# Optimization experiments

Measured on AMD Instinct MI355X. Metric: run time of the kernel, lower is better.

## Reference

```python
import jax, jax.numpy as jnp
import numpy as np

N_NODES = 100000
N_EDGES = 1600000
D_FEAT = 64


def setup_inputs() -> dict:
    key = jax.random.key(0)
    k1, k2 = jax.random.split(key)
    x = jax.random.normal(k1, (N_NODES, D_FEAT), dtype=jnp.float32)
    edge_index = jax.random.randint(k2, (2, N_EDGES), 0, N_NODES, dtype=jnp.int64)
    return {"x": x, "edge_index": edge_index}


def reference(x, edge_index):
    # LGConv with normalize=True: out = D^{-1/2} A D^{-1/2} x
    src, dst = edge_index[0], edge_index[1]
    n = x.shape[0]
    # in-degree at destination nodes
    deg = jax.ops.segment_sum(jnp.ones_like(dst, dtype=x.dtype), dst, num_segments=n)
    deg_inv_sqrt = jnp.where(deg > 0, jax.lax.rsqrt(jnp.maximum(deg, 1.0)), 0.0)
    # per-edge normalization, gather-scale-scatter
    norm = deg_inv_sqrt[src] * deg_inv_sqrt[dst]  # [E]
    msgs = x[src] * norm[:, None]                 # [E, D]
    out = jax.ops.segment_sum(msgs, dst, num_segments=n)  # [N, D]
    return out
```

## Files before the change

kernel.cpp:

```cpp
#include <hip/hip_runtime.h>
#include <hip/hip_fp16.h>


#define DFEAT 64
#define BIN_W 391
#define TILE 8192
#define K1_THREADS 256
#define EPT (TILE / K1_THREADS)
#define DIRW 257
#define K3_THREADS 1024
#define MAX_NT 512
#define CAP 8192

typedef unsigned long long u64;
typedef unsigned int u32;
typedef float f4v __attribute__((ext_vector_type(4)));

__global__ __launch_bounds__(K1_THREADS)
void bin_kernel(const int* __restrict__ src, const int* __restrict__ dst,
                u32* __restrict__ records, int* __restrict__ dir,
                int* __restrict__ bin_cnt, int E, int N) {
    __shared__ int cnt[256];
    __shared__ int off[DIRW];
    __shared__ int rnk[256];
    __shared__ u32 buf[TILE];

    const int t    = blockIdx.x;
    const int base = t * TILE;
    const int tid  = threadIdx.x;

    cnt[tid] = 0;
    rnk[tid] = 0;
    __syncthreads();

    u32 rec[EPT];
    int myb[EPT];
    #pragma unroll
    for (int i = 0; i < EPT; ++i) {
        int e = base + tid + i * K1_THREADS;
        int b = -1;
        u32 r = 0;
        if (e < E) {
            unsigned d = (unsigned)dst[e];
            unsigned s = (unsigned)src[e];
            if (d < (unsigned)N && s < (unsigned)N) {
                b = (int)(d / BIN_W);
                r = ((d - (unsigned)b * BIN_W) << 23) | s;
            }
        }
        myb[i] = b;
        rec[i] = r;
        if (b >= 0) atomicAdd(&cnt[b], 1);
    }
    __syncthreads();

    int v = cnt[tid];
    off[tid] = v;
    __syncthreads();
    for (int d = 1; d < 256; d <<= 1) {
        int add = (tid >= d) ? off[tid - d] : 0;
        __syncthreads();
        off[tid] += add;
        __syncthreads();
    }
    int incl = off[tid];
    __syncthreads();
    off[tid] = incl - v;
    if (tid == 255) off[256] = incl;
    __syncthreads();

    dir[t * DIRW + tid] = off[tid];
    if (tid == 0) dir[t * DIRW + 256] = off[256];
    if (v > 0) atomicAdd(&bin_cnt[tid], v);

    #pragma unroll
    for (int i = 0; i < EPT; ++i) {
        int b = myb[i];
        if (b >= 0) {
            int r = atomicAdd(&rnk[b], 1);
            buf[off[b] + r] = rec[i];
        }
    }
    __syncthreads();

    int total = off[256];
    for (int i = tid; i < total; i += K1_THREADS)
        records[(size_t)base + i] = buf[i];
}

__global__ __launch_bounds__(K3_THREADS)
void csr_build_kernel(const u32* __restrict__ records,
                      const int* __restrict__ dir,
                      const int* __restrict__ bin_cnt,
                      float* __restrict__ dis,
                      int* __restrict__ row_ptr,
                      int* __restrict__ csr_src, int N, int NT, int NB,
                      int bshift, int nbuckets) {
    __shared__ u32 ldsrec[CAP];
    __shared__ int deg[512];
    __shared__ int cur[BIN_W];
    __shared__ int sbeg[MAX_NT];
    __shared__ int send[MAX_NT];
    __shared__ int lofs[MAX_NT];
    __shared__ int sh_total, sh_gb0;

    const int b  = blockIdx.x;
    const int lo = b * BIN_W;
    const int nodes = min(BIN_W, N - lo);
    const int tid = threadIdx.x;
    const int wave = tid >> 6, lane = tid & 63;

    int bv = 0;
    if (tid < 512) { bv = (tid < NB) ? bin_cnt[tid] : 0; deg[tid] = bv; }
    __syncthreads();
    for (int d = 1; d < 512; d <<= 1) {
        int a = (tid < 512 && tid >= d) ? deg[tid - d] : 0;
        __syncthreads();
        if (tid < 512) deg[tid] += a;
        __syncthreads();
    }
    if (tid == b) sh_gb0 = deg[tid] - bv;
    if (b == 0 && tid == 0) row_ptr[N] = deg[NB - 1];
    __syncthreads();

    for (int t = tid; t < NT; t += K3_THREADS) {
        sbeg[t] = dir[t * DIRW + b];
        send[t] = dir[t * DIRW + b + 1];
    }
    __syncthreads();
    if (tid < 512) deg[tid] = (tid < NT) ? (send[tid] - sbeg[tid]) : 0;
    __syncthreads();
    for (int d = 1; d < 512; d <<= 1) {
        int a = (tid < 512 && tid >= d) ? deg[tid - d] : 0;
        __syncthreads();
        if (tid < 512) deg[tid] += a;
        __syncthreads();
    }
    if (tid < NT) lofs[tid] = deg[tid] - (send[tid] - sbeg[tid]);
    if (tid == 0) sh_total = deg[511];
    __syncthreads();

    const int total = sh_total;
    const bool fits = (total <= CAP);

    if (fits) {
        for (int rb = wave * 2; rb < NT; rb += 32) {
            int r = rb + (lane >> 5);
            if (r < NT) {
                int g0  = r * TILE + sbeg[r];
                int l0  = lofs[r];
                int len = send[r] - sbeg[r];
                for (int k = (lane & 31); k < len; k += 32)
                    ldsrec[l0 + k] = records[g0 + k];
            }
        }
    }
    __syncthreads();

    if (tid < 512) deg[tid] = 0;
    __syncthreads();
    if (fits) {
        for (int i = tid; i < total; i += K3_THREADS)
            atomicAdd(&deg[ldsrec[i] >> 23], 1);
    } else {
        for (int t = wave; t < NT; t += 16) {
            int s = sbeg[t], e = send[t], gb = t * TILE;
            for (int k = s + lane; k < e; k += 64)
                atomicAdd(&deg[records[gb + k] >> 23], 1);
        }
    }
    __syncthreads();

    if (tid < nodes) {
        int c = deg[tid];
        dis[lo + tid] = (c > 0) ? rsqrtf((float)c) : 0.0f;
    }

    int v0 = (tid < 512) ? deg[tid] : 0;
    __syncthreads();
    for (int d = 1; d < 512; d <<= 1) {
        int a = (tid < 512 && tid >= d) ? deg[tid - d] : 0;
        __syncthreads();
        if (tid < 512) deg[tid] += a;
        __syncthreads();
    }
    if (tid < nodes) {
        int g = sh_gb0 + deg[tid] - v0;
        row_ptr[lo + tid] = g;
        cur[tid] = g;
    }
    __syncthreads();

    if (fits) {
        for (int p = 0; p < nbuckets; ++p) {
            for (int i = tid; i < total; i += K3_THREADS) {
                u32 r = ldsrec[i];
                u32 s = r & 0x7FFFFF;
                if ((int)(s >> bshift) == p) {
                    int pos = atomicAdd(&cur[r >> 23], 1);
                    csr_src[pos] = (int)s;
                }
            }
            __syncthreads();
        }
    } else {
        for (int t = wave; t < NT; t += 16) {
            int s = sbeg[t], e = send[t], gb = t * TILE;
            for (int k = s + lane; k < e; k += 64) {
                u32 r = records[gb + k];
                int p = atomicAdd(&cur[r >> 23], 1);
                csr_src[p] = (int)(r & 0x7FFFFF);
            }
        }
    }
}

__global__ __launch_bounds__(256)
void stage_xs_kernel(const float* __restrict__ x, const float* __restrict__ dis,
                     __half2* __restrict__ xs, int total4 ) {
    int i = blockIdx.x * blockDim.x + threadIdx.x;
    if (i < total4) {
        float w = dis[i >> 4];
        float4 f = *reinterpret_cast<const float4*>(x + (size_t)i * 4);
        xs[i * 2]     = __floats2half2_rn(f.x * w, f.y * w);
        xs[i * 2 + 1] = __floats2half2_rn(f.z * w, f.w * w);
    }
}

struct alignas(8) h4 { __half2 a, b; };

__global__ void gather_s_kernel(const h4* __restrict__ xs4,
                                const int* __restrict__ row_ptr,
                                const int* __restrict__ csr_src,
                                const float* __restrict__ dis,
                                float* __restrict__ out, int N) {
    long long gt = blockIdx.x * (long long)blockDim.x + threadIdx.x;
    int node = (int)((gt >> 6) * 4) + ((threadIdx.x & 63) >> 4);
    int c8 = threadIdx.x & 15;
    if (node >= N) return;
    int beg = row_ptr[node];
    int end = row_ptr[node + 1];
    float a0 = 0.0f, a1 = 0.0f, a2 = 0.0f, a3 = 0.0f;
    int k = beg;
    for (; k + 1 < end; k += 2) {
        int s0 = csr_src[k];
        int s1 = csr_src[k + 1];
        h4 v0 = xs4[(size_t)s0 * 16 + c8];
        h4 v1 = xs4[(size_t)s1 * 16 + c8];
        float2 f00 = __half22float2(v0.a), f01 = __half22float2(v0.b);
        float2 f10 = __half22float2(v1.a), f11 = __half22float2(v1.b);
        a0 += f00.x + f10.x;
        a1 += f00.y + f10.y;
        a2 += f01.x + f11.x;
        a3 += f01.y + f11.y;
    }
    if (k < end) {
        int s0 = csr_src[k];
        h4 v0 = xs4[(size_t)s0 * 16 + c8];
        float2 f00 = __half22float2(v0.a), f01 = __half22float2(v0.b);
        a0 += f00.x; a1 += f00.y; a2 += f01.x; a3 += f01.y;
    }
    float dd = dis[node];
    f4v o = { a0 * dd, a1 * dd, a2 * dd, a3 * dd };
    __builtin_nontemporal_store(o, (f4v*)(out + (size_t)node * DFEAT + c8 * 4));
}

__global__ void fb_deg_kernel(const int* __restrict__ dst,
                              float* __restrict__ deg, int E, int N) {
    int e = blockIdx.x * blockDim.x + threadIdx.x;
    if (e < E) {
        unsigned d = (unsigned)dst[e];
        if (d < (unsigned)N) unsafeAtomicAdd(&deg[d], 1.0f);
    }
}
__global__ void fb_dis_kernel(float* __restrict__ deg, int N) {
    int i = blockIdx.x * blockDim.x + threadIdx.x;
    if (i < N) {
        float d = deg[i];
        deg[i] = (d > 0.0f) ? rsqrtf(d) : 0.0f;
    }
}
__global__ void fb_scatter_kernel(const float* __restrict__ x,
                                  const int* __restrict__ src,
                                  const int* __restrict__ dst,
                                  const float* __restrict__ dis,
                                  float* __restrict__ out, int E, int N) {
    long long t = (long long)blockIdx.x * blockDim.x + threadIdx.x;
    int e = (int)(t >> 4);
    int c = (int)(t & 15);
    if (e >= E) return;
    unsigned s = (unsigned)src[e];
    unsigned d = (unsigned)dst[e];
    if (s >= (unsigned)N || d >= (unsigned)N) return;
    float norm = dis[s] * dis[d];
    const float4 v = *reinterpret_cast<const float4*>(x + (size_t)s * DFEAT + c * 4);
    float* o = out + (size_t)d * DFEAT + c * 4;
    unsafeAtomicAdd(o + 0, v.x * norm);
    unsafeAtomicAdd(o + 1, v.y * norm);
    unsafeAtomicAdd(o + 2, v.z * norm);
    unsafeAtomicAdd(o + 3, v.w * norm);
}

extern "C" void kernel_launch(void* const* d_in, const int* in_sizes, int n_in,
                              void* d_out, int out_size, void* d_ws, size_t ws_size,
                              hipStream_t stream) {
    const float* x  = (const float*)d_in[0];
    const int*   ei = (const int*)d_in[1];

    const int N = in_sizes[0] / DFEAT;
    const int E = in_sizes[1] / 2;
    const int* src = ei;
    const int* dst = ei + E;

    float* out = (float*)d_out;

    const int NB = (N + BIN_W - 1) / BIN_W;
    const int NT = (E + TILE - 1) / TILE;

    int bshift = 13;
    while ((((N - 1) >> bshift) + 1) > 16) bshift++;
    int nbuckets = ((N - 1) >> bshift) + 1;

    char* base = (char*)d_ws;
    size_t off = 0;
    auto alloc = [&](size_t bytes) { void* p = base + off; off += (bytes + 15) & ~(size_t)15; return p; };
    size_t rec_bytes = (size_t)NT * TILE * 4;
    size_t xs_bytes  = (size_t)N * DFEAT * 2;
    size_t region    = rec_bytes > xs_bytes ? rec_bytes : xs_bytes;
    u32*   records  = (u32*)alloc(region);
    int*   dir      = (int*)alloc((size_t)NT * DIRW * 4);
    int*   bin_cnt  = (int*)alloc(256 * 4);
    float* dis      = (float*)alloc((size_t)N * 4);
    int*   row_ptr  = (int*)alloc((size_t)(N + 1) * 4);
    int*   csr_src  = (int*)alloc((size_t)E * 4);

    const bool ok = (off <= ws_size) && (NB <= 256) && (NT <= MAX_NT) &&
                    (N <= (1 << 23)) && (BIN_W <= 512);

    if (ok) {
        hipMemsetAsync(bin_cnt, 0, 256 * 4, stream);

        bin_kernel<<<NT, K1_THREADS, 0, stream>>>(src, dst, records, dir, bin_cnt, E, N);
        csr_build_kernel<<<NB, K3_THREADS, 0, stream>>>(records, dir, bin_cnt, dis,
                                                        row_ptr, csr_src, N, NT, NB,
                                                        bshift, nbuckets);

        __half2* xs = (__half2*)records;
        int total4 = N * DFEAT / 4;
        stage_xs_kernel<<<(total4 + 255) / 256, 256, 0, stream>>>(x, dis, xs, total4);

        int gblocks = (N + 15) / 16;
        gather_s_kernel<<<gblocks, 256, 0, stream>>>((const h4*)xs, row_ptr, csr_src, dis, out, N);
    } else {
        float* deg = (float*)d_ws;
        hipMemsetAsync(deg, 0, (size_t)N * 4, stream);
        hipMemsetAsync(out, 0, (size_t)out_size * 4, stream);
        int eb = (E + 255) / 256;
        fb_deg_kernel<<<eb, 256, 0, stream>>>(dst, deg, E, N);
        int nb = (N + 255) / 256;
        fb_dis_kernel<<<nb, 256, 0, stream>>>(deg, N);
        long long total = (long long)E * 16;
        int sb = (int)((total + 255) / 256);
        fb_scatter_kernel<<<sb, 256, 0, stream>>>(x, src, dst, deg, out, E, N);
    }
}
```

Before: 106.8 us.

## Replace multi-pass bucketed CSR scatter with single-pass composite-key counting sort

The CSR build used to make 16 passes over the LDS records, one per source bucket, to keep the source indices within each row roughly sorted. It now counts edges per (destination node, source bucket) key, scans all keys with a 1024-wide prefix sum, and scatters every edge in a single pass using the key offsets. This removes the repeated passes and their barriers, at the cost of a larger LDS counter array and a longer scan. The gather kernel is also unrolled to four edges per iteration, with nontemporal loads for the edge indices.

```diff
diff --git a/kernel.cpp b/kernel.cpp
--- a/kernel.cpp
+++ b/kernel.cpp
@@ -11,6 +11,9 @@
 #define K3_THREADS 1024
 #define MAX_NT 512
 #define CAP 8192
+#define NBUCK 16
+#define KMAXP (BIN_W * NBUCK)
+#define KPT ((KMAXP + K3_THREADS - 1) / K3_THREADS)
 
 typedef unsigned long long u64;
 typedef unsigned int u32;
@@ -95,10 +98,10 @@
                       float* __restrict__ dis,
                       int* __restrict__ row_ptr,
                       int* __restrict__ csr_src, int N, int NT, int NB,
-                      int bshift, int nbuckets) {
+                      int bshift) {
     __shared__ u32 ldsrec[CAP];
-    __shared__ int deg[512];
-    __shared__ int cur[BIN_W];
+    __shared__ int cnt2[KMAXP];
+    __shared__ int psum[K3_THREADS];
     __shared__ int sbeg[MAX_NT];
     __shared__ int send[MAX_NT];
     __shared__ int lofs[MAX_NT];
@@ -110,34 +113,35 @@
     const int tid = threadIdx.x;
     const int wave = tid >> 6, lane = tid & 63;
 
-    int bv = 0;
-    if (tid < 512) { bv = (tid < NB) ? bin_cnt[tid] : 0; deg[tid] = bv; }
-    __syncthreads();
-    for (int d = 1; d < 512; d <<= 1) {
-        int a = (tid < 512 && tid >= d) ? deg[tid - d] : 0;
-        __syncthreads();
-        if (tid < 512) deg[tid] += a;
-        __syncthreads();
-    }
-    if (tid == b) sh_gb0 = deg[tid] - bv;
-    if (b == 0 && tid == 0) row_ptr[N] = deg[NB - 1];
-    __syncthreads();
-
-    for (int t = tid; t < NT; t += K3_THREADS) {
-        sbeg[t] = dir[t * DIRW + b];
-        send[t] = dir[t * DIRW + b + 1];
-    }
-    __syncthreads();
-    if (tid < 512) deg[tid] = (tid < NT) ? (send[tid] - sbeg[tid]) : 0;
-    __syncthreads();
-    for (int d = 1; d < 512; d <<= 1) {
-        int a = (tid < 512 && tid >= d) ? deg[tid - d] : 0;
-        __syncthreads();
-        if (tid < 512) deg[tid] += a;
-        __syncthreads();
-    }
-    if (tid < NT) lofs[tid] = deg[tid] - (send[tid] - sbeg[tid]);
-    if (tid == 0) sh_total = deg[511];
+    int bv = (tid < NB) ? bin_cnt[tid] : 0;
+    psum[tid] = bv;
+    __syncthreads();
+    for (int d = 1; d < K3_THREADS; d <<= 1) {
+        int a = (tid >= d) ? psum[tid - d] : 0;
+        __syncthreads();
+        psum[tid] += a;
+        __syncthreads();
+    }
+    if (tid == b) sh_gb0 = psum[tid] - bv;
+    if (b == 0 && tid == NB - 1) row_ptr[N] = psum[tid];
+    __syncthreads();
+
+    int len = 0;
+    if (tid < NT) {
+        sbeg[tid] = dir[tid * DIRW + b];
+        send[tid] = dir[tid * DIRW + b + 1];
+        len = send[tid] - sbeg[tid];
+    }
+    psum[tid] = len;
+    __syncthreads();
+    for (int d = 1; d < K3_THREADS; d <<= 1) {
+        int a = (tid >= d) ? psum[tid - d] : 0;
+        __syncthreads();
+        psum[tid] += a;
+        __syncthreads();
+    }
+    if (tid < NT) lofs[tid] = psum[tid] - len;
+    if (tid == K3_THREADS - 1) sh_total = psum[tid];
     __syncthreads();
 
     const int total = sh_total;
@@ -149,67 +153,87 @@
             if (r < NT) {
                 int g0  = r * TILE + sbeg[r];
                 int l0  = lofs[r];
-                int len = send[r] - sbeg[r];
-                for (int k = (lane & 31); k < len; k += 32)
+                int ln  = send[r] - sbeg[r];
+                for (int k = (lane & 31); k < ln; k += 32)
                     ldsrec[l0 + k] = records[g0 + k];
             }
         }
     }
     __syncthreads();
 
-    if (tid < 512) deg[tid] = 0;
+    for (int i = tid; i < KMAXP; i += K3_THREADS) cnt2[i] = 0;
     __syncthreads();
     if (fits) {
-        for (int i = tid; i < total; i += K3_THREADS)
-            atomicAdd(&deg[ldsrec[i] >> 23], 1);
-    } else {
-        for (int t = wave; t < NT; t += 16) {
-            int s = sbeg[t], e = send[t], gb = t * TILE;
-            for (int k = s + lane; k < e; k += 64)
-                atomicAdd(&deg[records[gb + k] >> 23], 1);
-        }
-    }
-    __syncthreads();
-
-    if (tid < nodes) {
-        int c = deg[tid];
-        dis[lo + tid] = (c > 0) ? rsqrtf((float)c) : 0.0f;
-    }
-
-    int v0 = (tid < 512) ? deg[tid] : 0;
-    __syncthreads();
-    for (int d = 1; d < 512; d <<= 1) {
-        int a = (tid < 512 && tid >= d) ? deg[tid - d] : 0;
-        __syncthreads();
-        if (tid < 512) deg[tid] += a;
-        __syncthreads();
-    }
-    if (tid < nodes) {
-        int g = sh_gb0 + deg[tid] - v0;
-        row_ptr[lo + tid] = g;
-        cur[tid] = g;
-    }
-    __syncthreads();
-
-    if (fits) {
-        for (int p = 0; p < nbuckets; ++p) {
-            for (int i = tid; i < total; i += K3_THREADS) {
-                u32 r = ldsrec[i];
-                u32 s = r & 0x7FFFFF;
-                if ((int)(s >> bshift) == p) {
-                    int pos = atomicAdd(&cur[r >> 23], 1);
-                    csr_src[pos] = (int)s;
-                }
-            }
-            __syncthreads();
+        for (int i = tid; i < total; i += K3_THREADS) {
+            u32 r = ldsrec[i];
+            int key = (int)(r >> 23) * NBUCK + (int)((r & 0x7FFFFF) >> bshift);
+            atomicAdd(&cnt2[key], 1);
         }
     } else {
         for (int t = wave; t < NT; t += 16) {
             int s = sbeg[t], e = send[t], gb = t * TILE;
             for (int k = s + lane; k < e; k += 64) {
                 u32 r = records[gb + k];
-                int p = atomicAdd(&cur[r >> 23], 1);
-                csr_src[p] = (int)(r & 0x7FFFFF);
+                int key = (int)(r >> 23) * NBUCK + (int)((r & 0x7FFFFF) >> bshift);
+                atomicAdd(&cnt2[key], 1);
+            }
+        }
+    }
+    __syncthreads();
+
+    if (tid < nodes) {
+        int c = 0;
+        #pragma unroll
+        for (int j = 0; j < NBUCK; ++j) c += cnt2[tid * NBUCK + j];
+        dis[lo + tid] = (c > 0) ? rsqrtf((float)c) : 0.0f;
+    }
+
+    int base7 = tid * KPT;
+    int loc[KPT];
+    int s = 0;
+    #pragma unroll
+    for (int j = 0; j < KPT; ++j) {
+        int k = base7 + j;
+        loc[j] = s;
+        if (k < KMAXP) s += cnt2[k];
+    }
+    psum[tid] = s;
+    __syncthreads();
+    for (int d = 1; d < K3_THREADS; d <<= 1) {
+        int a = (tid >= d) ? psum[tid - d] : 0;
+        __syncthreads();
+        psum[tid] += a;
+        __syncthreads();
+    }
+    int excl = psum[tid] - s;
+    __syncthreads();
+    #pragma unroll
+    for (int j = 0; j < KPT; ++j) {
+        int k = base7 + j;
+        if (k < KMAXP) cnt2[k] = sh_gb0 + excl + loc[j];
+    }
+    __syncthreads();
+
+    if (tid < nodes) row_ptr[lo + tid] = cnt2[tid * NBUCK];
+    __syncthreads();
+
+    if (fits) {
+        for (int i = tid; i < total; i += K3_THREADS) {
+            u32 r = ldsrec[i];
+            u32 sc = r & 0x7FFFFF;
+            int key = (int)(r >> 23) * NBUCK + (int)(sc >> bshift);
+            int pos = atomicAdd(&cnt2[key], 1);
+            csr_src[pos] = (int)sc;
+        }
+    } else {
+        for (int t = wave; t < NT; t += 16) {
+            int s0 = sbeg[t], e0 = send[t], gb = t * TILE;
+            for (int k = s0 + lane; k < e0; k += 64) {
+                u32 r = records[gb + k];
+                u32 sc = r & 0x7FFFFF;
+                int key = (int)(r >> 23) * NBUCK + (int)(sc >> bshift);
+                int pos = atomicAdd(&cnt2[key], 1);
+                csr_src[pos] = (int)sc;
             }
         }
     }
@@ -242,20 +266,26 @@
     int end = row_ptr[node + 1];
     float a0 = 0.0f, a1 = 0.0f, a2 = 0.0f, a3 = 0.0f;
     int k = beg;
-    for (; k + 1 < end; k += 2) {
-        int s0 = csr_src[k];
-        int s1 = csr_src[k + 1];
+    for (; k + 3 < end; k += 4) {
+        int s0 = __builtin_nontemporal_load(csr_src + k);
+        int s1 = __builtin_nontemporal_load(csr_src + k + 1);
+        int s2 = __builtin_nontemporal_load(csr_src + k + 2);
+        int s3 = __builtin_nontemporal_load(csr_src + k + 3);
         h4 v0 = xs4[(size_t)s0 * 16 + c8];
         h4 v1 = xs4[(size_t)s1 * 16 + c8];
+        h4 v2 = xs4[(size_t)s2 * 16 + c8];
+        h4 v3 = xs4[(size_t)s3 * 16 + c8];
         float2 f00 = __half22float2(v0.a), f01 = __half22float2(v0.b);
         float2 f10 = __half22float2(v1.a), f11 = __half22float2(v1.b);
-        a0 += f00.x + f10.x;
-        a1 += f00.y + f10.y;
-        a2 += f01.x + f11.x;
-        a3 += f01.y + f11.y;
-    }
-    if (k < end) {
-        int s0 = csr_src[k];
+        float2 f20 = __half22float2(v2.a), f21 = __half22float2(v2.b);
+        float2 f30 = __half22float2(v3.a), f31 = __half22float2(v3.b);
+        a0 += (f00.x + f10.x) + (f20.x + f30.x);
+        a1 += (f00.y + f10.y) + (f20.y + f30.y);
+        a2 += (f01.x + f11.x) + (f21.x + f31.x);
+        a3 += (f01.y + f11.y) + (f21.y + f31.y);
+    }
+    for (; k < end; ++k) {
+        int s0 = __builtin_nontemporal_load(csr_src + k);
         h4 v0 = xs4[(size_t)s0 * 16 + c8];
         float2 f00 = __half22float2(v0.a), f01 = __half22float2(v0.b);
         a0 += f00.x; a1 += f00.y; a2 += f01.x; a3 += f01.y;
@@ -318,8 +348,7 @@
     const int NT = (E + TILE - 1) / TILE;
 
     int bshift = 13;
-    while ((((N - 1) >> bshift) + 1) > 16) bshift++;
-    int nbuckets = ((N - 1) >> bshift) + 1;
+    while ((((N - 1) >> bshift) + 1) > NBUCK) bshift++;
 
     char* base = (char*)d_ws;
     size_t off = 0;
@@ -335,7 +364,7 @@
     int*   csr_src  = (int*)alloc((size_t)E * 4);
 
     const bool ok = (off <= ws_size) && (NB <= 256) && (NT <= MAX_NT) &&
-                    (N <= (1 << 23)) && (BIN_W <= 512);
+                    (NT <= K3_THREADS) && (N <= (1 << 23)) && (BIN_W <= 512);
 
     if (ok) {
         hipMemsetAsync(bin_cnt, 0, 256 * 4, stream);
@@ -343,7 +372,7 @@
         bin_kernel<<<NT, K1_THREADS, 0, stream>>>(src, dst, records, dir, bin_cnt, E, N);
         csr_build_kernel<<<NB, K3_THREADS, 0, stream>>>(records, dir, bin_cnt, dis,
                                                         row_ptr, csr_src, N, NT, NB,
-                                                        bshift, nbuckets);
+                                                        bshift);
 
         __half2* xs = (__half2*)records;
         int total4 = N * DFEAT / 4;
```

Result: faster. 97.26 us (-8.9%).
